# Kernel optimization log

Hardware: AMD Instinct MI355X
Metric: run time of the kernel (lower is better)

## Reference

```python
import jax, jax.numpy as jnp
import numpy as np
import math

B, S, H = 512, 100, 1024
A, N = 128, 8
TAU = 1.0


def make_pe(seq_len, hidden):
    # PositionalEncoding buffer: pe[s, 0::2]=sin(pos*div), pe[s,1::2]=cos(pos*div)
    pos = jnp.arange(seq_len, dtype=jnp.float32)[:, None]          # [S,1]
    div = jnp.exp(jnp.arange(0, hidden, 2, dtype=jnp.float32) * (-math.log(10000.0) / hidden))
    pe = jnp.zeros((seq_len, hidden), dtype=jnp.float32)
    pe = pe.at[:, 0::2].set(jnp.sin(pos * div))
    pe = pe.at[:, 1::2].set(jnp.cos(pos * div))
    return pe                                                      # [S,H]


def setup_inputs() -> dict:
    key = jax.random.key(0)
    kx, kq, kk, kg = jax.random.split(key, 4)
    x = jax.random.normal(kx, (B, S, H), dtype=jnp.float32)
    # torch Linear weight layout: [out_features, in_features]
    Wq = jax.random.normal(kq, (A * N, H), dtype=jnp.float32) * (1.0 / math.sqrt(H))
    Wk = jax.random.normal(kk, (A * N, H), dtype=jnp.float32) * (1.0 / math.sqrt(H))
    # pre-sampled standard Gumbel noise (deterministic reference)
    u = jax.random.uniform(kg, (B * N, S), dtype=jnp.float32, minval=1e-6, maxval=1.0 - 1e-6)
    gumbel = -jnp.log(-jnp.log(u))
    return {"x": x, "Wq": Wq, "Wk": Wk, "gumbel": gumbel}


def reference(x, Wq, Wk, gumbel):
    b, s, h = x.shape
    pos_emb = x + make_pe(s, h)[None]                              # [B,S,H]
    Q = (pos_emb @ Wq.T).reshape(b, s, N, A).transpose(0, 2, 1, 3)  # [B,N,S,A]
    K = (pos_emb @ Wk.T).reshape(b, s, N, A).transpose(0, 2, 1, 3)  # [B,N,S,A]
    # original: sum_t (Q . K_t) / sqrt(H) / S  ==  Q . (sum_t K_t) / (sqrt(H)*S)
    Ksum = K.sum(axis=2)                                           # [B,N,A]
    logits = jnp.einsum('bnsa,bna->bns', Q, Ksum) / (math.sqrt(h) * s)
    y = (logits.reshape(b * N, s) + gumbel) / TAU
    soft = jax.nn.softmax(y, axis=-1)
    hard = jax.nn.one_hot(jnp.argmax(y, axis=-1), s, dtype=soft.dtype)
    # straight-through (forward value == hard one-hot)
    alphas = (hard - jax.lax.stop_gradient(soft) + soft).reshape(b, N, s)
    out = jnp.einsum('bns,bsh->bnh', alphas, x)                    # gather selected timesteps
    return out
```

## Files before the change

kernel.cpp:

```cpp
#include <hip/hip_runtime.h>
#include <float.h>
#include <math.h>

#define Bc 512
#define Sc 100
#define Hc 1024
#define Ac 128
#define Nc 8

__global__ __launch_bounds__(256) void pe_kernel(float* __restrict__ pe){
  int s = blockIdx.x;
  int t = threadIdx.x;
  const float fac = (float)(-9.210340371976184 / 1024.0);
  for(int i = t; i < Hc/2; i += 256){
    float div = expf((float)(2*i) * fac);
    float a = (float)s * div;
    pe[s*Hc + 2*i]     = sinf(a);
    pe[s*Hc + 2*i + 1] = cosf(a);
  }
}

__global__ __launch_bounds__(256) void pesum_kernel(const float* __restrict__ pe, float* __restrict__ pesum){
  int h = blockIdx.x*256 + threadIdx.x;
  float acc = 0.f;
  for(int s = 0; s < Sc; ++s) acc += pe[s*Hc + h];
  pesum[h] = acc;
}

__global__ __launch_bounds__(256) void xsum_kernel(const float* __restrict__ x, const float* __restrict__ pesum,
                                                   float* __restrict__ xsp){
  int b = blockIdx.x;
  int q = blockIdx.y;
  int t = threadIdx.x;
  const float4* xr = (const float4*)(x + (size_t)b*Sc*Hc);
  float4 acc;
  if(q == 0) acc = ((const float4*)pesum)[t];
  else       acc = make_float4(0.f,0.f,0.f,0.f);
  int s0 = q*25;
  #pragma unroll 5
  for(int s = s0; s < s0+25; ++s){
    float4 v = xr[s*(Hc/4) + t];
    acc.x += v.x; acc.y += v.y; acc.z += v.z; acc.w += v.w;
  }
  ((float4*)(xsp + ((size_t)b*4 + q)*Hc))[t] = acc;
}

__global__ __launch_bounds__(256) void ksum_gemm(const float* __restrict__ xs, const float* __restrict__ Wk,
                                                 float* __restrict__ Ksum){
  __shared__ float As[32][33];
  __shared__ float Bs[32][68];
  int t = threadIdx.x;
  int j0 = blockIdx.x*64, b0 = blockIdx.y*32;
  int bi = (t>>4)*2;
  int j4 = (t&15)*4;
  float acc[2][4] = {{0,0,0,0},{0,0,0,0}};
  int ra = t>>3, ca = t&7;
  for(int k0 = 0; k0 < Hc; k0 += 32){
    const float* xa = xs + (size_t)(b0+ra)*(4*Hc) + k0 + ca*4;
    float4 a4 = *(const float4*)(xa);
    float4 p1 = *(const float4*)(xa + Hc);
    float4 p2 = *(const float4*)(xa + 2*Hc);
    float4 p3 = *(const float4*)(xa + 3*Hc);
    a4.x += p1.x + p2.x + p3.x;
    a4.y += p1.y + p2.y + p3.y;
    a4.z += p1.z + p2.z + p3.z;
    a4.w += p1.w + p2.w + p3.w;
    As[ca*4+0][ra]=a4.x; As[ca*4+1][ra]=a4.y; As[ca*4+2][ra]=a4.z; As[ca*4+3][ra]=a4.w;
    #pragma unroll
    for(int ph = 0; ph < 2; ++ph){
      int q = t + ph*256;
      int r = q>>3, c = q&7;
      float4 b4 = *(const float4*)(Wk + (size_t)(j0+r)*Hc + k0 + c*4);
      Bs[c*4+0][r]=b4.x; Bs[c*4+1][r]=b4.y; Bs[c*4+2][r]=b4.z; Bs[c*4+3][r]=b4.w;
    }
    __syncthreads();
    #pragma unroll
    for(int kk = 0; kk < 32; ++kk){
      float a0 = As[kk][bi], a1 = As[kk][bi+1];
      float4 bq = *(const float4*)&Bs[kk][j4];
      acc[0][0]=fmaf(a0,bq.x,acc[0][0]); acc[0][1]=fmaf(a0,bq.y,acc[0][1]);
      acc[0][2]=fmaf(a0,bq.z,acc[0][2]); acc[0][3]=fmaf(a0,bq.w,acc[0][3]);
      acc[1][0]=fmaf(a1,bq.x,acc[1][0]); acc[1][1]=fmaf(a1,bq.y,acc[1][1]);
      acc[1][2]=fmaf(a1,bq.z,acc[1][2]); acc[1][3]=fmaf(a1,bq.w,acc[1][3]);
    }
    __syncthreads();
  }
  #pragma unroll
  for(int ii = 0; ii < 2; ++ii){
    float4 o = make_float4(acc[ii][0],acc[ii][1],acc[ii][2],acc[ii][3]);
    *(float4*)(Ksum + (size_t)(b0+bi+ii)*Hc + j0 + j4) = o;
  }
}

__global__ __launch_bounds__(256) void v_gemm(const float* __restrict__ Ksum, const float* __restrict__ Wq,
                                              float* __restrict__ v){
  __shared__ float As[32][33];
  __shared__ float Bs[32][68];
  int t = threadIdx.x;
  int h0 = blockIdx.x*64, b0 = blockIdx.y*32, n = blockIdx.z;
  int bi = (t>>4)*2;
  int j4 = (t&15)*4;
  float acc[2][4] = {{0,0,0,0},{0,0,0,0}};
  int ra = t>>3, ca = t&7;
  for(int k0 = 0; k0 < Ac; k0 += 32){
    float4 a4 = *(const float4*)(Ksum + (size_t)(b0+ra)*Hc + n*Ac + k0 + ca*4);
    As[ca*4+0][ra]=a4.x; As[ca*4+1][ra]=a4.y; As[ca*4+2][ra]=a4.z; As[ca*4+3][ra]=a4.w;
    #pragma unroll
    for(int ph = 0; ph < 2; ++ph){
      int q = t + ph*256;
      int r = q>>4, c = q&15;
      float4 b4 = *(const float4*)(Wq + (size_t)(n*Ac + k0 + r)*Hc + h0 + c*4);
      *(float4*)&Bs[r][c*4] = b4;
    }
    __syncthreads();
    #pragma unroll
    for(int kk = 0; kk < 32; ++kk){
      float a0 = As[kk][bi], a1 = As[kk][bi+1];
      float4 bq = *(const float4*)&Bs[kk][j4];
      acc[0][0]=fmaf(a0,bq.x,acc[0][0]); acc[0][1]=fmaf(a0,bq.y,acc[0][1]);
      acc[0][2]=fmaf(a0,bq.z,acc[0][2]); acc[0][3]=fmaf(a0,bq.w,acc[0][3]);
      acc[1][0]=fmaf(a1,bq.x,acc[1][0]); acc[1][1]=fmaf(a1,bq.y,acc[1][1]);
      acc[1][2]=fmaf(a1,bq.z,acc[1][2]); acc[1][3]=fmaf(a1,bq.w,acc[1][3]);
    }
    __syncthreads();
  }
  #pragma unroll
  for(int ii = 0; ii < 2; ++ii){
    float4 o = make_float4(acc[ii][0],acc[ii][1],acc[ii][2],acc[ii][3]);
    *(float4*)(v + ((size_t)(b0+bi+ii)*Nc + n)*Hc + h0 + j4) = o;
  }
}

__global__ __launch_bounds__(1024) void attn_kernel(const float* __restrict__ x, const float* __restrict__ pe,
                                                    const float* __restrict__ v, const float* __restrict__ g,
                                                    float* __restrict__ out){
  __shared__ float4 tile[1600];
  __shared__ float part[8][Nc][104];
  __shared__ int sidx[Nc];
  const int b = blockIdx.x;
  const int t = threadIdx.x;
  const int lane = t & 63;
  const int w  = __builtin_amdgcn_readfirstlane(t >> 6);
  const int kq = w & 7, sh = w >> 3;

  const int r1 = t >> 4, c1 = t & 15;
  const bool has2 = (t < 576);
  const int e2 = t + 1024;
  const int r2 = e2 >> 4, c2 = e2 & 15;

  const float* xb = x + (size_t)b*Sc*Hc;
  const float* vb = v + (size_t)b*Nc*Hc;

  int rw = sh*64 + lane;
  int r  = (rw < Sc) ? rw : (Sc-1);
  const bool valid = (rw < Sc);

  float acc[Nc];
  #pragma unroll
  for(int n = 0; n < Nc; ++n) acc[n] = 0.f;

  float4 xv1 = *(const float4*)(xb + r1*Hc + c1*4);
  float4 pv1 = *(const float4*)(pe + r1*Hc + c1*4);
  float4 xv2 = make_float4(0,0,0,0), pv2 = make_float4(0,0,0,0);
  if(has2){ xv2 = *(const float4*)(xb + r2*Hc + c2*4);
            pv2 = *(const float4*)(pe + r2*Hc + c2*4); }

  for(int kt = 0; kt < 16; ++kt){
    __syncthreads();
    tile[r1*16 + (c1 ^ (r1&7))] = make_float4(xv1.x+pv1.x, xv1.y+pv1.y, xv1.z+pv1.z, xv1.w+pv1.w);
    if(has2)
      tile[r2*16 + (c2 ^ (r2&7))] = make_float4(xv2.x+pv2.x, xv2.y+pv2.y, xv2.z+pv2.z, xv2.w+pv2.w);
    if(kt < 15){
      int ko = (kt+1)*64;
      xv1 = *(const float4*)(xb + r1*Hc + ko + c1*4);
      pv1 = *(const float4*)(pe + r1*Hc + ko + c1*4);
      if(has2){ xv2 = *(const float4*)(xb + r2*Hc + ko + c2*4);
                pv2 = *(const float4*)(pe + r2*Hc + ko + c2*4); }
    }
    __syncthreads();
    #pragma unroll
    for(int j = 0; j < 2; ++j){
      float4 xe = tile[r*16 + ((kq*2 + j) ^ (r&7))];
      const float* vk = vb + kt*64 + kq*8 + j*4;
      #pragma unroll
      for(int n = 0; n < Nc; ++n){
        const float* vn = vk + n*Hc;
        acc[n] = fmaf(xe.x, vn[0], acc[n]);
        acc[n] = fmaf(xe.y, vn[1], acc[n]);
        acc[n] = fmaf(xe.z, vn[2], acc[n]);
        acc[n] = fmaf(xe.w, vn[3], acc[n]);
      }
    }
  }
  if(valid){
    #pragma unroll
    for(int n = 0; n < Nc; ++n) part[kq][n][rw] = acc[n];
  }
  __syncthreads();

  if(w < Nc){
    int n = w, j = lane;
    float best = -FLT_MAX; int bidx = 0;
    #pragma unroll
    for(int i = 0; i < 2; ++i){
      int s2 = j + 64*i;
      if(s2 < Sc){
        float dot = 0.f;
        #pragma unroll
        for(int q = 0; q < 8; ++q) dot += part[q][n][s2];
        float y = dot/3200.0f + g[(size_t)(b*Nc + n)*Sc + s2];
        if(y > best){ best = y; bidx = s2; }
      }
    }
    #pragma unroll
    for(int m = 32; m >= 1; m >>= 1){
      float ob = __shfl_xor(best, m, 64);
      int   oi = __shfl_xor(bidx, m, 64);
      if(ob > best || (ob == best && oi < bidx)){ best = ob; bidx = oi; }
    }
    if(j == 0) sidx[n] = bidx;
  }
  __syncthreads();

  const float4* xb4 = (const float4*)xb;
  float4* ob4 = (float4*)(out + (size_t)b*Nc*Hc);
  #pragma unroll
  for(int i = 0; i < 2; ++i){
    int idx = i*1024 + t;
    int nn = idx >> 8, c = idx & 255;
    ob4[idx] = xb4[sidx[nn]*256 + c];
  }
}

extern "C" void kernel_launch(void* const* d_in, const int* in_sizes, int n_in,
                              void* d_out, int out_size, void* d_ws, size_t ws_size,
                              hipStream_t stream) {
  const float* x  = (const float*)d_in[0];
  const float* Wq = (const float*)d_in[1];
  const float* Wk = (const float*)d_in[2];
  const float* g  = (const float*)d_in[3];
  float* out = (float*)d_out;

  char* ws = (char*)d_ws;
  float* pe    = (float*)(ws);
  float* pesum = (float*)(ws +    409600);
  float* xsp   = (float*)(ws +    413696);
  float* Ksum  = (float*)(ws +   8802304);
  float* v     = (float*)(ws +  10899456);

  pe_kernel   <<<100, 256, 0, stream>>>(pe);
  pesum_kernel<<<4,   256, 0, stream>>>(pe, pesum);
  xsum_kernel <<<dim3(512,4),   256, 0, stream>>>(x, pesum, xsp);
  ksum_gemm   <<<dim3(16,16),   256, 0, stream>>>(xsp, Wk, Ksum);
  v_gemm      <<<dim3(16,16,8), 256, 0, stream>>>(Ksum, Wq, v);
  attn_kernel <<<512, 1024, 0, stream>>>(x, pe, v, g, out);
}
```

Measured before the change: 154.5 us.

## Rewrite Ksum and V GEMMs with wave-uniform scalar weight loads and split-K

Replaces the two shared-memory tiled GEMMs with kernels where each wave reads a wave-uniform slice of the weight matrix (which the compiler can load via scalar loads) and each lane owns one batch row, with activations staged in XOR-swizzled LDS. Wk is transposed by a new per-call kernel so weight rows are contiguous along the output dimension. The Ksum GEMM is split along K into two partial buffers, which the V GEMM sums on load. This removes LDS staging of weights and raises block count, at the cost of an extra transpose launch, more workspace and extra partial-sum traffic.

```diff
diff --git a/kernel.cpp b/kernel.cpp
--- a/kernel.cpp
+++ b/kernel.cpp
@@ -25,6 +25,19 @@
   float acc = 0.f;
   for(int s = 0; s < Sc; ++s) acc += pe[s*Hc + h];
   pesum[h] = acc;
+}
+
+__global__ __launch_bounds__(256) void wkT_kernel(const float* __restrict__ Wk, float* __restrict__ WkT){
+  __shared__ float tl[32][33];
+  int bx = blockIdx.x, by = blockIdx.y;
+  int tx = threadIdx.x & 31, ty = threadIdx.x >> 5;
+  #pragma unroll
+  for(int i = 0; i < 4; ++i)
+    tl[ty + i*8][tx] = Wk[(size_t)(by*32 + ty + i*8)*Hc + bx*32 + tx];
+  __syncthreads();
+  #pragma unroll
+  for(int i = 0; i < 4; ++i)
+    WkT[(size_t)(bx*32 + ty + i*8)*Hc + by*32 + tx] = tl[tx][ty + i*8];
 }
 
 __global__ __launch_bounds__(256) void xsum_kernel(const float* __restrict__ x, const float* __restrict__ pesum,
@@ -45,90 +58,87 @@
   ((float4*)(xsp + ((size_t)b*4 + q)*Hc))[t] = acc;
 }
 
-__global__ __launch_bounds__(256) void ksum_gemm(const float* __restrict__ xs, const float* __restrict__ Wk,
-                                                 float* __restrict__ Ksum){
-  __shared__ float As[32][33];
-  __shared__ float Bs[32][68];
-  int t = threadIdx.x;
-  int j0 = blockIdx.x*64, b0 = blockIdx.y*32;
-  int bi = (t>>4)*2;
-  int j4 = (t&15)*4;
-  float acc[2][4] = {{0,0,0,0},{0,0,0,0}};
-  int ra = t>>3, ca = t&7;
-  for(int k0 = 0; k0 < Hc; k0 += 32){
-    const float* xa = xs + (size_t)(b0+ra)*(4*Hc) + k0 + ca*4;
-    float4 a4 = *(const float4*)(xa);
-    float4 p1 = *(const float4*)(xa + Hc);
-    float4 p2 = *(const float4*)(xa + 2*Hc);
-    float4 p3 = *(const float4*)(xa + 3*Hc);
-    a4.x += p1.x + p2.x + p3.x;
-    a4.y += p1.y + p2.y + p3.y;
-    a4.z += p1.z + p2.z + p3.z;
-    a4.w += p1.w + p2.w + p3.w;
-    As[ca*4+0][ra]=a4.x; As[ca*4+1][ra]=a4.y; As[ca*4+2][ra]=a4.z; As[ca*4+3][ra]=a4.w;
-    #pragma unroll
-    for(int ph = 0; ph < 2; ++ph){
-      int q = t + ph*256;
-      int r = q>>3, c = q&7;
-      float4 b4 = *(const float4*)(Wk + (size_t)(j0+r)*Hc + k0 + c*4);
-      Bs[c*4+0][r]=b4.x; Bs[c*4+1][r]=b4.y; Bs[c*4+2][r]=b4.z; Bs[c*4+3][r]=b4.w;
-    }
-    __syncthreads();
-    #pragma unroll
-    for(int kk = 0; kk < 32; ++kk){
-      float a0 = As[kk][bi], a1 = As[kk][bi+1];
-      float4 bq = *(const float4*)&Bs[kk][j4];
-      acc[0][0]=fmaf(a0,bq.x,acc[0][0]); acc[0][1]=fmaf(a0,bq.y,acc[0][1]);
-      acc[0][2]=fmaf(a0,bq.z,acc[0][2]); acc[0][3]=fmaf(a0,bq.w,acc[0][3]);
-      acc[1][0]=fmaf(a1,bq.x,acc[1][0]); acc[1][1]=fmaf(a1,bq.y,acc[1][1]);
-      acc[1][2]=fmaf(a1,bq.z,acc[1][2]); acc[1][3]=fmaf(a1,bq.w,acc[1][3]);
-    }
-    __syncthreads();
-  }
-  #pragma unroll
-  for(int ii = 0; ii < 2; ++ii){
-    float4 o = make_float4(acc[ii][0],acc[ii][1],acc[ii][2],acc[ii][3]);
-    *(float4*)(Ksum + (size_t)(b0+bi+ii)*Hc + j0 + j4) = o;
-  }
-}
-
-__global__ __launch_bounds__(256) void v_gemm(const float* __restrict__ Ksum, const float* __restrict__ Wq,
-                                              float* __restrict__ v){
-  __shared__ float As[32][33];
-  __shared__ float Bs[32][68];
-  int t = threadIdx.x;
-  int h0 = blockIdx.x*64, b0 = blockIdx.y*32, n = blockIdx.z;
-  int bi = (t>>4)*2;
-  int j4 = (t&15)*4;
-  float acc[2][4] = {{0,0,0,0},{0,0,0,0}};
-  int ra = t>>3, ca = t&7;
+__global__ __launch_bounds__(256) void ksum_scalar(const float* __restrict__ xsp, const float* __restrict__ WkT,
+                                                   float* __restrict__ Ksum2){
+  __shared__ float4 As[64][8];
+  int t = threadIdx.x;
+  int lane = t & 63;
+  int w  = __builtin_amdgcn_readfirstlane(t >> 6);
+  int b0 = blockIdx.y * 64;
+  int j0 = blockIdx.x * 32 + w * 8;
+  int ks = blockIdx.z;
+  float acc[8] = {0,0,0,0,0,0,0,0};
+  int rb = t & 63, kc = t >> 6;
+
+  for(int k0 = ks*512; k0 < ks*512 + 512; k0 += 32){
+    const float* xa = xsp + (size_t)(b0+rb)*(4*Hc) + k0 + kc*8;
+    float4 sa = *(const float4*)(xa),       sb = *(const float4*)(xa+4);
+    #pragma unroll
+    for(int q = 1; q < 4; ++q){
+      float4 qa = *(const float4*)(xa + q*Hc), qb = *(const float4*)(xa + q*Hc + 4);
+      sa.x += qa.x; sa.y += qa.y; sa.z += qa.z; sa.w += qa.w;
+      sb.x += qb.x; sb.y += qb.y; sb.z += qb.z; sb.w += qb.w;
+    }
+    __syncthreads();
+    As[rb][(kc*2+0) ^ (rb&7)] = sa;
+    As[rb][(kc*2+1) ^ (rb&7)] = sb;
+    __syncthreads();
+    #pragma unroll
+    for(int kc4 = 0; kc4 < 8; ++kc4){
+      float4 a4 = As[lane][kc4 ^ (lane&7)];
+      const float* wr = WkT + (size_t)(k0 + kc4*4)*Hc + j0;
+      #pragma unroll
+      for(int kk = 0; kk < 4; ++kk){
+        float av = (kk==0)?a4.x:(kk==1)?a4.y:(kk==2)?a4.z:a4.w;
+        const float* wk = wr + kk*Hc;
+        #pragma unroll
+        for(int j = 0; j < 8; ++j) acc[j] = fmaf(av, wk[j], acc[j]);
+      }
+    }
+  }
+  float* cp = Ksum2 + ((size_t)ks*Bc + b0 + lane)*Hc + j0;
+  *(float4*)cp     = make_float4(acc[0],acc[1],acc[2],acc[3]);
+  *(float4*)(cp+4) = make_float4(acc[4],acc[5],acc[6],acc[7]);
+}
+
+__global__ __launch_bounds__(256) void v_scalar(const float* __restrict__ Ksum2, const float* __restrict__ Wq,
+                                                float* __restrict__ v){
+  __shared__ float4 As[64][8];
+  int t = threadIdx.x;
+  int lane = t & 63;
+  int w  = __builtin_amdgcn_readfirstlane(t >> 6);
+  int b0 = blockIdx.y * 64;
+  int h0 = blockIdx.x * 32 + w * 8;
+  int n  = blockIdx.z;
+  float acc[8] = {0,0,0,0,0,0,0,0};
+  int rb = t & 63, kc = t >> 6;
+
   for(int k0 = 0; k0 < Ac; k0 += 32){
-    float4 a4 = *(const float4*)(Ksum + (size_t)(b0+ra)*Hc + n*Ac + k0 + ca*4);
-    As[ca*4+0][ra]=a4.x; As[ca*4+1][ra]=a4.y; As[ca*4+2][ra]=a4.z; As[ca*4+3][ra]=a4.w;
-    #pragma unroll
-    for(int ph = 0; ph < 2; ++ph){
-      int q = t + ph*256;
-      int r = q>>4, c = q&15;
-      float4 b4 = *(const float4*)(Wq + (size_t)(n*Ac + k0 + r)*Hc + h0 + c*4);
-      *(float4*)&Bs[r][c*4] = b4;
-    }
-    __syncthreads();
-    #pragma unroll
-    for(int kk = 0; kk < 32; ++kk){
-      float a0 = As[kk][bi], a1 = As[kk][bi+1];
-      float4 bq = *(const float4*)&Bs[kk][j4];
-      acc[0][0]=fmaf(a0,bq.x,acc[0][0]); acc[0][1]=fmaf(a0,bq.y,acc[0][1]);
-      acc[0][2]=fmaf(a0,bq.z,acc[0][2]); acc[0][3]=fmaf(a0,bq.w,acc[0][3]);
-      acc[1][0]=fmaf(a1,bq.x,acc[1][0]); acc[1][1]=fmaf(a1,bq.y,acc[1][1]);
-      acc[1][2]=fmaf(a1,bq.z,acc[1][2]); acc[1][3]=fmaf(a1,bq.w,acc[1][3]);
-    }
-    __syncthreads();
-  }
-  #pragma unroll
-  for(int ii = 0; ii < 2; ++ii){
-    float4 o = make_float4(acc[ii][0],acc[ii][1],acc[ii][2],acc[ii][3]);
-    *(float4*)(v + ((size_t)(b0+bi+ii)*Nc + n)*Hc + h0 + j4) = o;
-  }
+    const float* ka = Ksum2 + (size_t)(b0+rb)*Hc + n*Ac + k0 + kc*8;
+    float4 sa = *(const float4*)(ka),                 sb = *(const float4*)(ka+4);
+    float4 qa = *(const float4*)(ka + (size_t)Bc*Hc), qb = *(const float4*)(ka + (size_t)Bc*Hc + 4);
+    sa.x += qa.x; sa.y += qa.y; sa.z += qa.z; sa.w += qa.w;
+    sb.x += qb.x; sb.y += qb.y; sb.z += qb.z; sb.w += qb.w;
+    __syncthreads();
+    As[rb][(kc*2+0) ^ (rb&7)] = sa;
+    As[rb][(kc*2+1) ^ (rb&7)] = sb;
+    __syncthreads();
+    #pragma unroll
+    for(int kc4 = 0; kc4 < 8; ++kc4){
+      float4 a4 = As[lane][kc4 ^ (lane&7)];
+      const float* wr = Wq + (size_t)(n*Ac + k0 + kc4*4)*Hc + h0;
+      #pragma unroll
+      for(int kk = 0; kk < 4; ++kk){
+        float av = (kk==0)?a4.x:(kk==1)?a4.y:(kk==2)?a4.z:a4.w;
+        const float* wk = wr + kk*Hc;
+        #pragma unroll
+        for(int j = 0; j < 8; ++j) acc[j] = fmaf(av, wk[j], acc[j]);
+      }
+    }
+  }
+  float* cp = v + ((size_t)(b0+lane)*Nc + n)*Hc + h0;
+  *(float4*)cp     = make_float4(acc[0],acc[1],acc[2],acc[3]);
+  *(float4*)(cp+4) = make_float4(acc[4],acc[5],acc[6],acc[7]);
 }
 
 __global__ __launch_bounds__(1024) void attn_kernel(const float* __restrict__ x, const float* __restrict__ pe,
@@ -245,13 +255,15 @@
   float* pe    = (float*)(ws);
   float* pesum = (float*)(ws +    409600);
   float* xsp   = (float*)(ws +    413696);
-  float* Ksum  = (float*)(ws +   8802304);
-  float* v     = (float*)(ws +  10899456);
+  float* Ksum2 = (float*)(ws +   8802304);
+  float* v     = (float*)(ws +  12996608);
+  float* WkT   = (float*)(ws +  29773824);
 
   pe_kernel   <<<100, 256, 0, stream>>>(pe);
   pesum_kernel<<<4,   256, 0, stream>>>(pe, pesum);
+  wkT_kernel  <<<dim3(32,32),   256, 0, stream>>>(Wk, WkT);
   xsum_kernel <<<dim3(512,4),   256, 0, stream>>>(x, pesum, xsp);
-  ksum_gemm   <<<dim3(16,16),   256, 0, stream>>>(xsp, Wk, Ksum);
-  v_gemm      <<<dim3(16,16,8), 256, 0, stream>>>(Ksum, Wq, v);
+  ksum_scalar <<<dim3(32,8,2),  256, 0, stream>>>(xsp, WkT, Ksum2);
+  v_scalar    <<<dim3(32,8,8),  256, 0, stream>>>(Ksum2, Wq, v);
   attn_kernel <<<512, 1024, 0, stream>>>(x, pe, v, g, out);
 }
```

Result: slower. 206.9 us (+33.9%).

## Retile Ksum and V GEMMs to 64x128 tiles with split-K and register prefetch

Applied to the files above, without the earlier changes.

Replaces the two small-tile FP32 GEMMs with 64x128 block tiles computing 4x8 outputs per thread, raising arithmetic intensity per shared-memory load. The Ksum GEMM is split four ways over K, with a separate reduction kernel. The partial x sums are now pre-reduced by their own kernel rather than inside the GEMM. Global loads are staged through registers before the shared-memory stores, which gives some latency overlap. This adds two extra launches and extra global traffic for the split-K partials, and the workspace is reused by aliasing Ksum4 onto xsp.

```diff
diff --git a/kernel.cpp b/kernel.cpp
--- a/kernel.cpp
+++ b/kernel.cpp
@@ -7,6 +7,8 @@
 #define Hc 1024
 #define Ac 128
 #define Nc 8
+#define AS_ST 68
+#define BS_ST 132
 
 __global__ __launch_bounds__(256) void pe_kernel(float* __restrict__ pe){
   int s = blockIdx.x;
@@ -45,89 +47,155 @@
   ((float4*)(xsp + ((size_t)b*4 + q)*Hc))[t] = acc;
 }
 
-__global__ __launch_bounds__(256) void ksum_gemm(const float* __restrict__ xs, const float* __restrict__ Wk,
-                                                 float* __restrict__ Ksum){
-  __shared__ float As[32][33];
-  __shared__ float Bs[32][68];
-  int t = threadIdx.x;
-  int j0 = blockIdx.x*64, b0 = blockIdx.y*32;
-  int bi = (t>>4)*2;
-  int j4 = (t&15)*4;
-  float acc[2][4] = {{0,0,0,0},{0,0,0,0}};
-  int ra = t>>3, ca = t&7;
-  for(int k0 = 0; k0 < Hc; k0 += 32){
-    const float* xa = xs + (size_t)(b0+ra)*(4*Hc) + k0 + ca*4;
-    float4 a4 = *(const float4*)(xa);
-    float4 p1 = *(const float4*)(xa + Hc);
-    float4 p2 = *(const float4*)(xa + 2*Hc);
-    float4 p3 = *(const float4*)(xa + 3*Hc);
-    a4.x += p1.x + p2.x + p3.x;
-    a4.y += p1.y + p2.y + p3.y;
-    a4.z += p1.z + p2.z + p3.z;
-    a4.w += p1.w + p2.w + p3.w;
-    As[ca*4+0][ra]=a4.x; As[ca*4+1][ra]=a4.y; As[ca*4+2][ra]=a4.z; As[ca*4+3][ra]=a4.w;
-    #pragma unroll
-    for(int ph = 0; ph < 2; ++ph){
-      int q = t + ph*256;
-      int r = q>>3, c = q&7;
-      float4 b4 = *(const float4*)(Wk + (size_t)(j0+r)*Hc + k0 + c*4);
-      Bs[c*4+0][r]=b4.x; Bs[c*4+1][r]=b4.y; Bs[c*4+2][r]=b4.z; Bs[c*4+3][r]=b4.w;
-    }
-    __syncthreads();
-    #pragma unroll
+__global__ __launch_bounds__(256) void xsred_kernel(const float* __restrict__ xsp, float* __restrict__ xs){
+  int b = blockIdx.x, t = threadIdx.x;
+  const float4* p = (const float4*)(xsp + (size_t)b*4*Hc);
+  float4 a = p[t], b1 = p[256+t], c = p[512+t], d = p[768+t];
+  a.x += b1.x + c.x + d.x;
+  a.y += b1.y + c.y + d.y;
+  a.z += b1.z + c.z + d.z;
+  a.w += b1.w + c.w + d.w;
+  ((float4*)(xs + (size_t)b*Hc))[t] = a;
+}
+
+__global__ __launch_bounds__(256) void ksum_gemm2(const float* __restrict__ xs, const float* __restrict__ Wk,
+                                                  float* __restrict__ Ksum4){
+  __shared__ float As[32*AS_ST];
+  __shared__ float Bs[32*BS_ST];
+  const int t = threadIdx.x;
+  const int j0 = blockIdx.x*128, b0 = blockIdx.y*64, ks = blockIdx.z;
+  const int ty = t>>4, tx = t&15;
+  float acc[4][8];
+  #pragma unroll
+  for(int i = 0; i < 4; ++i)
+    #pragma unroll
+    for(int j = 0; j < 8; ++j) acc[i][j] = 0.f;
+
+  const int mA = (t>>3) & 63;
+  for(int k0 = ks*256; k0 < ks*256 + 256; k0 += 32){
+    float4 af[2], bf[4];
+    #pragma unroll
+    for(int i = 0; i < 2; ++i){
+      int id = t + i*256; int m = id>>3, q = id&7;
+      af[i] = *(const float4*)(xs + ((size_t)(b0+m)<<10) + k0 + q*4);
+    }
+    #pragma unroll
+    for(int i = 0; i < 4; ++i){
+      int id = t + i*256; int r = id>>3, c = id&7;
+      bf[i] = *(const float4*)(Wk + ((size_t)(j0+r)<<10) + k0 + c*4);
+    }
+    __syncthreads();
+    #pragma unroll
+    for(int i = 0; i < 2; ++i){
+      int id = t + i*256; int m = id>>3, q = id&7;
+      As[(q*4+0)*AS_ST + m] = af[i].x;
+      As[(q*4+1)*AS_ST + m] = af[i].y;
+      As[(q*4+2)*AS_ST + m] = af[i].z;
+      As[(q*4+3)*AS_ST + m] = af[i].w;
+    }
+    #pragma unroll
+    for(int i = 0; i < 4; ++i){
+      int id = t + i*256; int r = id>>3, c = id&7;
+      Bs[(c*4+0)*BS_ST + r] = bf[i].x;
+      Bs[(c*4+1)*BS_ST + r] = bf[i].y;
+      Bs[(c*4+2)*BS_ST + r] = bf[i].z;
+      Bs[(c*4+3)*BS_ST + r] = bf[i].w;
+    }
+    __syncthreads();
+    #pragma unroll 8
     for(int kk = 0; kk < 32; ++kk){
-      float a0 = As[kk][bi], a1 = As[kk][bi+1];
-      float4 bq = *(const float4*)&Bs[kk][j4];
-      acc[0][0]=fmaf(a0,bq.x,acc[0][0]); acc[0][1]=fmaf(a0,bq.y,acc[0][1]);
-      acc[0][2]=fmaf(a0,bq.z,acc[0][2]); acc[0][3]=fmaf(a0,bq.w,acc[0][3]);
-      acc[1][0]=fmaf(a1,bq.x,acc[1][0]); acc[1][1]=fmaf(a1,bq.y,acc[1][1]);
-      acc[1][2]=fmaf(a1,bq.z,acc[1][2]); acc[1][3]=fmaf(a1,bq.w,acc[1][3]);
-    }
-    __syncthreads();
-  }
-  #pragma unroll
-  for(int ii = 0; ii < 2; ++ii){
-    float4 o = make_float4(acc[ii][0],acc[ii][1],acc[ii][2],acc[ii][3]);
-    *(float4*)(Ksum + (size_t)(b0+bi+ii)*Hc + j0 + j4) = o;
-  }
-}
-
-__global__ __launch_bounds__(256) void v_gemm(const float* __restrict__ Ksum, const float* __restrict__ Wq,
-                                              float* __restrict__ v){
-  __shared__ float As[32][33];
-  __shared__ float Bs[32][68];
-  int t = threadIdx.x;
-  int h0 = blockIdx.x*64, b0 = blockIdx.y*32, n = blockIdx.z;
-  int bi = (t>>4)*2;
-  int j4 = (t&15)*4;
-  float acc[2][4] = {{0,0,0,0},{0,0,0,0}};
-  int ra = t>>3, ca = t&7;
+      float4 a4 = *(const float4*)&As[kk*AS_ST + ty*4];
+      float4 bu = *(const float4*)&Bs[kk*BS_ST + tx*4];
+      float4 bv = *(const float4*)&Bs[kk*BS_ST + 64 + tx*4];
+      float a[4] = {a4.x, a4.y, a4.z, a4.w};
+      float bb[8] = {bu.x,bu.y,bu.z,bu.w, bv.x,bv.y,bv.z,bv.w};
+      #pragma unroll
+      for(int i = 0; i < 4; ++i)
+        #pragma unroll
+        for(int j = 0; j < 8; ++j)
+          acc[i][j] = fmaf(a[i], bb[j], acc[i][j]);
+    }
+  }
+  (void)mA;
+  #pragma unroll
+  for(int i = 0; i < 4; ++i){
+    float* cp = Ksum4 + (((size_t)ks*Bc + b0 + ty*4 + i)<<10) + j0 + tx*4;
+    *(float4*)cp        = make_float4(acc[i][0],acc[i][1],acc[i][2],acc[i][3]);
+    *(float4*)(cp + 64) = make_float4(acc[i][4],acc[i][5],acc[i][6],acc[i][7]);
+  }
+}
+
+__global__ __launch_bounds__(256) void ksred_kernel(const float* __restrict__ Ksum4, float* __restrict__ Ksum){
+  int b = blockIdx.x, t = threadIdx.x;
+  const float4* p = (const float4*)(Ksum4 + ((size_t)b<<10));
+  const size_t sl = (size_t)Bc*Hc/4;
+  float4 a = p[t], b1 = p[sl+t], c = p[2*sl+t], d = p[3*sl+t];
+  a.x += b1.x + c.x + d.x;
+  a.y += b1.y + c.y + d.y;
+  a.z += b1.z + c.z + d.z;
+  a.w += b1.w + c.w + d.w;
+  ((float4*)(Ksum + ((size_t)b<<10)))[t] = a;
+}
+
+__global__ __launch_bounds__(256) void v_gemm2(const float* __restrict__ Ksum, const float* __restrict__ Wq,
+                                               float* __restrict__ v){
+  __shared__ float As[32*AS_ST];
+  __shared__ float Bs[32*BS_ST];
+  const int t = threadIdx.x;
+  const int h0 = blockIdx.x*128, b0 = blockIdx.y*64, n = blockIdx.z;
+  const int ty = t>>4, tx = t&15;
+  float acc[4][8];
+  #pragma unroll
+  for(int i = 0; i < 4; ++i)
+    #pragma unroll
+    for(int j = 0; j < 8; ++j) acc[i][j] = 0.f;
+
   for(int k0 = 0; k0 < Ac; k0 += 32){
-    float4 a4 = *(const float4*)(Ksum + (size_t)(b0+ra)*Hc + n*Ac + k0 + ca*4);
-    As[ca*4+0][ra]=a4.x; As[ca*4+1][ra]=a4.y; As[ca*4+2][ra]=a4.z; As[ca*4+3][ra]=a4.w;
-    #pragma unroll
-    for(int ph = 0; ph < 2; ++ph){
-      int q = t + ph*256;
-      int r = q>>4, c = q&15;
-      float4 b4 = *(const float4*)(Wq + (size_t)(n*Ac + k0 + r)*Hc + h0 + c*4);
-      *(float4*)&Bs[r][c*4] = b4;
-    }
-    __syncthreads();
-    #pragma unroll
+    float4 af[2], bf[4];
+    #pragma unroll
+    for(int i = 0; i < 2; ++i){
+      int id = t + i*256; int m = id>>3, q = id&7;
+      af[i] = *(const float4*)(Ksum + ((size_t)(b0+m)<<10) + n*Ac + k0 + q*4);
+    }
+    #pragma unroll
+    for(int i = 0; i < 4; ++i){
+      int id = t + i*256; int kk = id>>5, q = id&31;
+      bf[i] = *(const float4*)(Wq + ((size_t)(n*Ac + k0 + kk)<<10) + h0 + q*4);
+    }
+    __syncthreads();
+    #pragma unroll
+    for(int i = 0; i < 2; ++i){
+      int id = t + i*256; int m = id>>3, q = id&7;
+      As[(q*4+0)*AS_ST + m] = af[i].x;
+      As[(q*4+1)*AS_ST + m] = af[i].y;
+      As[(q*4+2)*AS_ST + m] = af[i].z;
+      As[(q*4+3)*AS_ST + m] = af[i].w;
+    }
+    #pragma unroll
+    for(int i = 0; i < 4; ++i){
+      int id = t + i*256; int kk = id>>5, q = id&31;
+      *(float4*)&Bs[kk*BS_ST + q*4] = bf[i];
+    }
+    __syncthreads();
+    #pragma unroll 8
     for(int kk = 0; kk < 32; ++kk){
-      float a0 = As[kk][bi], a1 = As[kk][bi+1];
-      float4 bq = *(const float4*)&Bs[kk][j4];
-      acc[0][0]=fmaf(a0,bq.x,acc[0][0]); acc[0][1]=fmaf(a0,bq.y,acc[0][1]);
-      acc[0][2]=fmaf(a0,bq.z,acc[0][2]); acc[0][3]=fmaf(a0,bq.w,acc[0][3]);
-      acc[1][0]=fmaf(a1,bq.x,acc[1][0]); acc[1][1]=fmaf(a1,bq.y,acc[1][1]);
-      acc[1][2]=fmaf(a1,bq.z,acc[1][2]); acc[1][3]=fmaf(a1,bq.w,acc[1][3]);
-    }
-    __syncthreads();
-  }
-  #pragma unroll
-  for(int ii = 0; ii < 2; ++ii){
-    float4 o = make_float4(acc[ii][0],acc[ii][1],acc[ii][2],acc[ii][3]);
-    *(float4*)(v + ((size_t)(b0+bi+ii)*Nc + n)*Hc + h0 + j4) = o;
+      float4 a4 = *(const float4*)&As[kk*AS_ST + ty*4];
+      float4 bu = *(const float4*)&Bs[kk*BS_ST + tx*4];
+      float4 bv = *(const float4*)&Bs[kk*BS_ST + 64 + tx*4];
+      float a[4] = {a4.x, a4.y, a4.z, a4.w};
+      float bb[8] = {bu.x,bu.y,bu.z,bu.w, bv.x,bv.y,bv.z,bv.w};
+      #pragma unroll
+      for(int i = 0; i < 4; ++i)
+        #pragma unroll
+        for(int j = 0; j < 8; ++j)
+          acc[i][j] = fmaf(a[i], bb[j], acc[i][j]);
+    }
+  }
+  #pragma unroll
+  for(int i = 0; i < 4; ++i){
+    float* cp = v + (((size_t)(b0 + ty*4 + i)*Nc + n)<<10) + h0 + tx*4;
+    *(float4*)cp        = make_float4(acc[i][0],acc[i][1],acc[i][2],acc[i][3]);
+    *(float4*)(cp + 64) = make_float4(acc[i][4],acc[i][5],acc[i][6],acc[i][7]);
   }
 }
 
@@ -245,13 +313,17 @@
   float* pe    = (float*)(ws);
   float* pesum = (float*)(ws +    409600);
   float* xsp   = (float*)(ws +    413696);
-  float* Ksum  = (float*)(ws +   8802304);
-  float* v     = (float*)(ws +  10899456);
+  float* Ksum4 = (float*)(ws +    413696);
+  float* xs    = (float*)(ws +   8802304);
+  float* Ksum  = (float*)(ws +  10899456);
+  float* v     = (float*)(ws +  12996608);
 
   pe_kernel   <<<100, 256, 0, stream>>>(pe);
   pesum_kernel<<<4,   256, 0, stream>>>(pe, pesum);
-  xsum_kernel <<<dim3(512,4),   256, 0, stream>>>(x, pesum, xsp);
-  ksum_gemm   <<<dim3(16,16),   256, 0, stream>>>(xsp, Wk, Ksum);
-  v_gemm      <<<dim3(16,16,8), 256, 0, stream>>>(Ksum, Wq, v);
+  xsum_kernel <<<dim3(512,4), 256, 0, stream>>>(x, pesum, xsp);
+  xsred_kernel<<<512, 256, 0, stream>>>(xsp, xs);
+  ksum_gemm2  <<<dim3(8,8,4), 256, 0, stream>>>(xs, Wk, Ksum4);
+  ksred_kernel<<<512, 256, 0, stream>>>(Ksum4, Ksum);
+  v_gemm2     <<<dim3(8,8,8), 256, 0, stream>>>(Ksum, Wq, v);
   attn_kernel <<<512, 1024, 0, stream>>>(x, pe, v, g, out);
 }
```

Result: faster. 146.4 us (-5.3%).
